# Kernel optimization log

Measured on AMD Instinct MI355X. Metric: run time of the kernel, lower is better.

The kernel has to match this reference:

```python
import jax, jax.numpy as jnp
import numpy as np

B, WIN, DM, DG, K = 32, 128, 1024, 64, 15  # batch, win_size(node feat dim), d_model(#nodes), graph embed, top_k


def setup_inputs() -> dict:
    key = jax.random.key(0)
    ks = jax.random.split(key, 7)
    sc_in = 1.0 / np.sqrt(WIN)
    return {
        "x": jax.random.normal(ks[0], (B, WIN, DM), jnp.float32),
        "Wq": jax.random.normal(ks[1], (DG, WIN), jnp.float32) * sc_in,
        "bq": jax.random.normal(ks[2], (DG,), jnp.float32) * 0.02,
        "Wk": jax.random.normal(ks[3], (DG, WIN), jnp.float32) * sc_in,
        "bk": jax.random.normal(ks[4], (DG,), jnp.float32) * 0.02,
        "Wg": jax.random.normal(ks[5], (WIN, WIN), jnp.float32) * sc_in,  # GCNConv lin weight [out,in]
        "bg": jax.random.normal(ks[6], (WIN,), jnp.float32) * 0.02,
    }


def _gcn_one(nf, Wq, bq, Wk, bk, Wg, bg):
    # nf: [N, F] node features (N = d_model, F = win_size)
    N = nf.shape[0]
    q = nf @ Wq.T + bq                      # [N, DG]
    k = nf @ Wk.T + bk                      # [N, DG]
    scores = (q @ k.T) * (1.0 / np.sqrt(DG))  # [N, N]
    scores = jnp.where(jnp.eye(N, dtype=bool), -jnp.inf, scores)
    _, tgt = jax.lax.top_k(scores, K)       # [N, K] top-k neighbors per source node
    src = jnp.repeat(jnp.arange(N), K)      # [N*K]
    tgt = tgt.reshape(-1)                   # [N*K]
    loops = jnp.arange(N)
    # manual self loops (module) + self loops added internally by GCNConv (default add_self_loops=True)
    src_all = jnp.concatenate([src, loops, loops])
    tgt_all = jnp.concatenate([tgt, loops, loops])
    # gcn_norm: degree over target (col) with unit edge weights
    deg = jax.ops.segment_sum(jnp.ones_like(tgt_all, jnp.float32), tgt_all, num_segments=N)
    dinv = jnp.where(deg > 0, jax.lax.rsqrt(deg), 0.0)
    norm = dinv[src_all] * dinv[tgt_all]    # [E]
    h = nf @ Wg.T                           # [N, F] linear transform (no bias inside lin)
    msg = h[src_all] * norm[:, None]        # gather + scale
    out = jax.ops.segment_sum(msg, tgt_all, num_segments=N) + bg  # scatter-add + bias
    return out                              # [N, F]


def reference(x, Wq, bq, Wk, bk, Wg, bg):
    # x: [B, win_size, d_model] -> nodes: [B, d_model, win_size]
    nodes = x.transpose(0, 2, 1)
    h = jax.vmap(lambda nf: _gcn_one(nf, Wq, bq, Wk, bk, Wg, bg))(nodes)  # [B, N, F]
    # n_layers == 1: no ReLU/dropout applied after last layer
    return h.transpose(0, 2, 1)  # [B, win_size, d_model]
```

## Files before the change

kernel.cpp:

```cpp
#include <hip/hip_runtime.h>

#define NBATCH 32
#define NN     1024
#define NF     128
#define NDG    64
#define TOPK   15

#define OFF_QH    ((size_t)0)
#define OFF_QL    ((size_t)4194304)
#define OFF_KH    ((size_t)8388608)
#define OFF_KL    ((size_t)12582912)
#define OFF_H     ((size_t)16777216)
#define OFF_DEG   ((size_t)33554432)
#define OFF_BMP   ((size_t)33685504)
#define OFF_WL    ((size_t)37879808)
#define OFF_TOPK  ((size_t)38010880)
#define OFF_W64   ((size_t)40108032)
#define OFF_QT64  ((size_t)40239104)
#define OFF_KT64  ((size_t)57016320)
#define OFF_TMP   ((size_t)0)

typedef short s8v  __attribute__((ext_vector_type(8)));
typedef float f4v  __attribute__((ext_vector_type(4)));
typedef unsigned short us8v __attribute__((ext_vector_type(8)));

__device__ inline unsigned short bf16_rne(float f) {
    unsigned u = __float_as_uint(f);
    return (unsigned short)((u + 0x7FFFu + ((u >> 16) & 1u)) >> 16);
}
__device__ inline float bf16_tof(unsigned short h) { return __uint_as_float(((unsigned)h) << 16); }

__device__ inline unsigned pack22(float s) {
    unsigned u   = __float_as_uint(s);
    int      mag = (int)(u & 0x7FFFFFFFu);
    int      t   = mag - 0x38800000;
    t = t < 0 ? 0 : (t > 0x07FFFFFF ? 0x07FFFFFF : t);
    unsigned ts = (unsigned)t >> 6;
    return ((int)u < 0) ? (0x1FFFFFu - ts) : (0x200000u | ts);
}
__device__ inline float dec22(unsigned val22) {
    bool pos = (val22 & 0x200000u) != 0;
    unsigned ts = pos ? (val22 & 0x1FFFFFu) : (0x1FFFFFu - (val22 & 0x1FFFFFu));
    float f = __uint_as_float((ts << 6) + 0x38800000u);
    return pos ? f : -f;
}

__global__ __launch_bounds__(256) void k_upcast(const float* __restrict__ Wq,
                                                const float* __restrict__ Wk,
                                                double* __restrict__ Wq64,
                                                double* __restrict__ Wk64) {
    int i = blockIdx.x * 256 + threadIdx.x;
    Wq64[i] = (double)Wq[i];
    Wk64[i] = (double)Wk[i];
}

__global__ __launch_bounds__(256) void k_prep(
    const float* __restrict__ x, const float* __restrict__ bq, const float* __restrict__ bk,
    const double* __restrict__ Wq64, const double* __restrict__ Wk64,
    const float* __restrict__ Wg,
    unsigned short* __restrict__ qh, unsigned short* __restrict__ ql,
    unsigned short* __restrict__ kh, unsigned short* __restrict__ kl,
    double* __restrict__ qT64, double* __restrict__ kT64,
    float* __restrict__ h,
    uint4* __restrict__ zbase, int zn)
{
    __shared__ float xs[64 * 129];
    const int t = threadIdx.x;
    const int l = t & 63;
    const int w = t >> 6;
    const int uw = __builtin_amdgcn_readfirstlane(w);
    const int n0 = blockIdx.x * 64;
    const int half = blockIdx.y;
    const int b  = blockIdx.z;

    {
        int lid = ((b * 2 + half) * 16 + blockIdx.x) * 256 + t;
        for (int i = lid; i < zn; i += 262144)
            zbase[i] = make_uint4(0u, 0u, 0u, 0u);
    }

    {
        const int j = t & 63, fg = t >> 6;
        for (int ff = 0; ff < 32; ++ff) {
            int f = fg + ff * 4;
            xs[j * 129 + f] = x[((size_t)b * NF + f) * NN + n0 + j];
        }
    }
    __syncthreads();

    {
        const int d0 = half * 32 + uw * 8;
        double accq[8], acck[8];
        #pragma unroll
        for (int dd = 0; dd < 8; ++dd) {
            accq[dd] = (double)bq[d0 + dd];
            acck[dd] = (double)bk[d0 + dd];
        }
        for (int fc = 0; fc < 32; ++fc) {
            double dx0 = (double)xs[l * 129 + fc * 4 + 0];
            double dx1 = (double)xs[l * 129 + fc * 4 + 1];
            double dx2 = (double)xs[l * 129 + fc * 4 + 2];
            double dx3 = (double)xs[l * 129 + fc * 4 + 3];
            #pragma unroll
            for (int dd = 0; dd < 8; ++dd) {
                int d = d0 + dd;
                const double* wq = &Wq64[d * NF + fc * 4];
                const double* wk = &Wk64[d * NF + fc * 4];
                accq[dd] += dx0 * wq[0] + dx1 * wq[1] + dx2 * wq[2] + dx3 * wq[3];
                acck[dd] += dx0 * wk[0] + dx1 * wk[1] + dx2 * wk[2] + dx3 * wk[3];
            }
        }
        #pragma unroll
        for (int dd = 0; dd < 8; ++dd) {
            size_t idx = ((size_t)b * NDG + d0 + dd) * NN + n0 + l;
            qT64[idx] = accq[dd];
            kT64[idx] = acck[dd];
        }
        us8v qh0, ql0, kh0, kl0;
        #pragma unroll
        for (int dd = 0; dd < 8; ++dd) {
            float fq = (float)accq[dd];
            unsigned short h1 = bf16_rne(fq);
            unsigned short l1 = bf16_rne(fq - bf16_tof(h1));
            float fk = (float)acck[dd];
            unsigned short h2 = bf16_rne(fk);
            unsigned short l2 = bf16_rne(fk - bf16_tof(h2));
            qh0[dd] = h1; ql0[dd] = l1; kh0[dd] = h2; kl0[dd] = l2;
        }
        size_t nb = ((size_t)b * NN + n0 + l) * NDG + d0;
        *(us8v*)&qh[nb] = qh0;
        *(us8v*)&ql[nb] = ql0;
        *(us8v*)&kh[nb] = kh0;
        *(us8v*)&kl[nb] = kl0;
    }

    {
        const int fp0 = half * 64 + uw * 16;
        float acc[16];
        #pragma unroll
        for (int i = 0; i < 16; ++i) acc[i] = 0.f;
        for (int fc = 0; fc < 32; ++fc) {
            float x0 = xs[l * 129 + fc * 4 + 0];
            float x1 = xs[l * 129 + fc * 4 + 1];
            float x2 = xs[l * 129 + fc * 4 + 2];
            float x3 = xs[l * 129 + fc * 4 + 3];
            #pragma unroll
            for (int ff = 0; ff < 16; ++ff) {
                const float* wg = &Wg[(fp0 + ff) * NF + fc * 4];
                acc[ff] += x0 * wg[0] + x1 * wg[1] + x2 * wg[2] + x3 * wg[3];
            }
        }
        __syncthreads();
        #pragma unroll
        for (int ff = 0; ff < 16; ++ff) xs[l * 129 + fp0 + ff] = acc[ff];
        __syncthreads();
        for (int r = 0; r < 16; ++r) {
            int idx = t + 256 * r;
            int n = idx >> 6, f = idx & 63;
            h[((size_t)b * NN + n0 + n) * NF + half * 64 + f] = xs[n * 129 + half * 64 + f];
        }
    }
}

__device__ inline unsigned bsort64(unsigned v, int l) {
    #pragma unroll
    for (int k = 2; k <= 64; k <<= 1) {
        #pragma unroll
        for (int j = k >> 1; j >= 1; j >>= 1) {
            unsigned pv = (unsigned)__shfl_xor((int)v, j, 64);
            bool tm = ((l & k) == 0) == ((l & j) == 0);
            unsigned hi = v > pv ? v : pv;
            unsigned lo = v > pv ? pv : v;
            v = tm ? hi : lo;
        }
    }
    return v;
}

__device__ inline void bsort64_2(unsigned& va, unsigned& vb, int l) {
    #pragma unroll
    for (int k = 2; k <= 64; k <<= 1) {
        #pragma unroll
        for (int j = k >> 1; j >= 1; j >>= 1) {
            unsigned pa = (unsigned)__shfl_xor((int)va, j, 64);
            unsigned pb = (unsigned)__shfl_xor((int)vb, j, 64);
            bool tm = ((l & k) == 0) == ((l & j) == 0);
            unsigned ha = va > pa ? va : pa, la = va > pa ? pa : va;
            unsigned hb = vb > pb ? vb : pb, lb = vb > pb ? pb : vb;
            va = tm ? ha : la;
            vb = tm ? hb : lb;
        }
    }
}

__global__ __launch_bounds__(512, 6) void k_score(
    const unsigned short* __restrict__ qh, const unsigned short* __restrict__ ql,
    const unsigned short* __restrict__ kh, const unsigned short* __restrict__ kl,
    const float* __restrict__ bk,
    int* __restrict__ deg, unsigned int* __restrict__ bmp,
    int* __restrict__ topk, int* __restrict__ wl_cnt, int* __restrict__ wl)
{
    __shared__ __align__(16) unsigned slots[16 * 256];
    __shared__ unsigned rowflag[16];
    const int t = threadIdx.x, l = t & 63, w = t >> 6;
    const int b = blockIdx.y, row0 = blockIdx.x * 16;
    const int m = l & 15, q4 = l >> 4;

    {
        uint4* z = (uint4*)slots;
        z[t]       = make_uint4(0u, 0u, 0u, 0u);
        z[t + 512] = make_uint4(0u, 0u, 0u, 0u);
        if (t < 16) rowflag[t] = 0u;
    }

    size_t abase = ((size_t)b * NN + row0 + m) * NDG + q4 * 8;
    s8v ah0 = *(const s8v*)&qh[abase];
    s8v ah1 = *(const s8v*)&qh[abase + 32];
    s8v al0 = *(const s8v*)&ql[abase];
    s8v al1 = *(const s8v*)&ql[abase + 32];

    unsigned Trow[4];
    {
        float ssq = 0.f, smn = 0.f;
        #pragma unroll
        for (int j = 0; j < 8; ++j) {
            float q0 = bf16_tof(((us8v)ah0)[j]) + bf16_tof(((us8v)al0)[j]);
            float q1 = bf16_tof(((us8v)ah1)[j]) + bf16_tof(((us8v)al1)[j]);
            float b0 = bk[q4 * 8 + j];
            float b1 = bk[q4 * 8 + 32 + j];
            ssq += q0 * q0 + q1 * q1;
            smn += q0 * b0 + q1 * b1;
        }
        ssq += __shfl_xor(ssq, 16, 64); ssq += __shfl_xor(ssq, 32, 64);
        smn += __shfl_xor(smn, 16, 64); smn += __shfl_xor(smn, 32, 64);
        float t_m = 0.125f * smn + 0.2125f * __builtin_sqrtf(ssq);
        unsigned Tm = pack22(t_m) << 10;
        #pragma unroll
        for (int r = 0; r < 4; ++r)
            Trow[r] = (unsigned)__shfl((int)Tm, 4 * q4 + r, 64);
    }
    __syncthreads();

    const int colbase = w * 128;
    unsigned basec[4] = {0u, 0u, 0u, 0u};
    #pragma unroll
    for (int tt = 0; tt < 8; ++tt) {
        int col = colbase + tt * 16 + m;
        size_t bbase = ((size_t)b * NN + col) * NDG + q4 * 8;
        s8v bh0 = *(const s8v*)&kh[bbase];
        s8v bh1 = *(const s8v*)&kh[bbase + 32];
        s8v bl0 = *(const s8v*)&kl[bbase];
        s8v bl1 = *(const s8v*)&kl[bbase + 32];
        f4v acc = {0.f, 0.f, 0.f, 0.f};
        acc = __builtin_amdgcn_mfma_f32_16x16x32_bf16(al0, bl0, acc, 0, 0, 0);
        acc = __builtin_amdgcn_mfma_f32_16x16x32_bf16(al1, bl1, acc, 0, 0, 0);
        acc = __builtin_amdgcn_mfma_f32_16x16x32_bf16(ah0, bl0, acc, 0, 0, 0);
        acc = __builtin_amdgcn_mfma_f32_16x16x32_bf16(ah1, bl1, acc, 0, 0, 0);
        acc = __builtin_amdgcn_mfma_f32_16x16x32_bf16(al0, bh0, acc, 0, 0, 0);
        acc = __builtin_amdgcn_mfma_f32_16x16x32_bf16(al1, bh1, acc, 0, 0, 0);
        acc = __builtin_amdgcn_mfma_f32_16x16x32_bf16(ah0, bh0, acc, 0, 0, 0);
        acc = __builtin_amdgcn_mfma_f32_16x16x32_bf16(ah1, bh1, acc, 0, 0, 0);
        #pragma unroll
        for (int r = 0; r < 4; ++r) {
            int row  = q4 * 4 + r;
            int grow = row0 + row;
            float s = acc[r] * 0.125f;
            unsigned c22 = (col == grow) ? 0u : pack22(s);
            unsigned v = (c22 << 10) | (unsigned)(1023 - col);
            bool p = v >= Trow[r];
            unsigned long long mk = __ballot(p);
            unsigned w16 = (unsigned)(mk >> (q4 * 16)) & 0xFFFFu;
            unsigned idx = basec[r] + (unsigned)__popc(w16 & ((1u << m) - 1u));
            if (p && idx < 32u) slots[row * 256 + w * 32 + (int)idx] = v;
            basec[r] += (unsigned)__popc(w16);
        }
    }
    #pragma unroll
    for (int r = 0; r < 4; ++r)
        if (m == 0 && basec[r] > 32u) rowflag[q4 * 4 + r] = 1u;
    __syncthreads();

    const int rA = 2 * w, rB = 2 * w + 1;
    uint4 ca = *(const uint4*)&slots[rA * 256 + l * 4];
    uint4 cb = *(const uint4*)&slots[rB * 256 + l * 4];

    unsigned mxa = ca.x > ca.y ? ca.x : ca.y;  mxa = mxa > ca.z ? mxa : ca.z;  mxa = mxa > ca.w ? mxa : ca.w;
    unsigned mxb = cb.x > cb.y ? cb.x : cb.y;  mxb = mxb > cb.z ? mxb : cb.z;  mxb = mxb > cb.w ? mxb : cb.w;
    bsort64_2(mxa, mxb, l);
    unsigned Ta = (unsigned)__shfl((int)mxa, 15, 64);
    unsigned Tb = (unsigned)__shfl((int)mxb, 15, 64);

    int ka0 = (ca.x >= Ta && ca.x) ? 1 : 0, ka1 = (ca.y >= Ta && ca.y) ? 1 : 0;
    int ka2 = (ca.z >= Ta && ca.z) ? 1 : 0, ka3 = (ca.w >= Ta && ca.w) ? 1 : 0;
    int kb0 = (cb.x >= Tb && cb.x) ? 1 : 0, kb1 = (cb.y >= Tb && cb.y) ? 1 : 0;
    int kb2 = (cb.z >= Tb && cb.z) ? 1 : 0, kb3 = (cb.w >= Tb && cb.w) ? 1 : 0;
    int cntA = ka0 + ka1 + ka2 + ka3;
    int cntB = kb0 + kb1 + kb2 + kb3;
    int preA = cntA, preB = cntB;
    #pragma unroll
    for (int d = 1; d < 64; d <<= 1) {
        int oA = __shfl_up(preA, d, 64);
        int oB = __shfl_up(preB, d, 64);
        if (l >= d) { preA += oA; preB += oB; }
    }
    const int CA = __shfl(preA, 63, 64);
    const int CB = __shfl(preB, 63, 64);

    {
        unsigned* scr = &slots[rA * 256];
        int off = preA - cntA;
        if (ka0) scr[off++] = ca.x;
        if (ka1) scr[off++] = ca.y;
        if (ka2) scr[off++] = ca.z;
        if (ka3) scr[off++] = ca.w;
    }
    {
        unsigned* scr = &slots[rB * 256];
        int off = preB - cntB;
        if (kb0) scr[off++] = cb.x;
        if (kb1) scr[off++] = cb.y;
        if (kb2) scr[off++] = cb.z;
        if (kb3) scr[off++] = cb.w;
    }
    unsigned cva = (l < CA && l < 64) ? slots[rA * 256 + l] : 0u;
    unsigned cvb = (l < CB && l < 64) ? slots[rB * 256 + l] : 0u;
    bsort64_2(cva, cvb, l);

    #pragma unroll
    for (int rr = 0; rr < 2; ++rr) {
        const int row  = rr == 0 ? rA : rB;
        const int grow = row0 + row;
        unsigned res   = rr == 0 ? cva : cvb;
        const int C2   = rr == 0 ? CA : CB;

        unsigned r14 = (unsigned)__shfl((int)res, 14, 64);
        unsigned r15 = (unsigned)__shfl((int)res, 15, 64);
        bool fb = (rowflag[row] != 0u) || (C2 > 64) || (r15 == 0u);

        bool flagged;
        if (fb) {
            flagged = true;
        } else {
            float s15 = dec22(r14 >> 10), s16 = dec22(r15 >> 10);
            unsigned e15 = (__float_as_uint(fabsf(s15)) >> 23) & 255u;
            unsigned e16 = (__float_as_uint(fabsf(s16)) >> 23) & 255u;
            unsigned e = e15 > e16 ? e15 : e16;
            float qq = __uint_as_float((e - 17) << 23);
            flagged = (s15 - s16) < (4.f * qq + 1e-4f);
        }
        if (l < 15) {
            int col = fb ? ((grow + 1 + l) & 1023)
                         : (1023 - (int)(res & 1023u));
            atomicAdd(&deg[b * NN + col], 1);
            atomicOr(&bmp[((size_t)b * NN + col) * 32 + (grow >> 5)], 1u << (grow & 31));
            if (flagged) topk[(b * NN + grow) * 16 + l] = col;
        }
        if (l == 0 && flagged) {
            int idx = atomicAdd(wl_cnt, 1);
            if (idx < 32767) wl[idx] = b * NN + grow;
        }
    }
}

__global__ __launch_bounds__(64) void k_repair(
    const double* __restrict__ qT64, const double* __restrict__ kT64,
    const int* __restrict__ topk, const int* __restrict__ wl_cnt, const int* __restrict__ wl,
    int* __restrict__ deg, unsigned int* __restrict__ bmp)
{
    const int l = threadIdx.x;
    __shared__ double qld[64];
    __shared__ int oldset[15], newset[15];
    const double NEGINF = -__builtin_inf();
    int n = wl_cnt[0]; if (n > 32767) n = 32767;

    for (int i = blockIdx.x; i < n; i += 1024) {
        int rg = wl[i];
        int b = rg >> 10, row = rg & 1023;

        __syncthreads();
        qld[l] = qT64[((size_t)b * NDG + l) * NN + row];
        if (l < 15) oldset[l] = topk[(b * NN + row) * 16 + l];
        __syncthreads();

        double sc[16];
        #pragma unroll
        for (int tt = 0; tt < 16; ++tt) sc[tt] = 0.0;
        const double* kb = &kT64[(size_t)b * NDG * NN];
        double buf[16];
        #pragma unroll
        for (int tt = 0; tt < 16; ++tt) buf[tt] = kb[l + 64 * tt];
        for (int d = 0; d < 64; ++d) {
            double nb[16];
            if (d < 63) {
                const double* kr = kb + (size_t)(d + 1) * NN;
                #pragma unroll
                for (int tt = 0; tt < 16; ++tt) nb[tt] = kr[l + 64 * tt];
            }
            double qd = qld[d];
            #pragma unroll
            for (int tt = 0; tt < 16; ++tt) sc[tt] += qd * buf[tt];
            if (d < 63) {
                #pragma unroll
                for (int tt = 0; tt < 16; ++tt) buf[tt] = nb[tt];
            }
        }
        #pragma unroll
        for (int tt = 0; tt < 16; ++tt) if (l + 64 * tt == row) sc[tt] = NEGINF;

        for (int it = 0; it < 15; ++it) {
            double lv = NEGINF; int lc = 0x7fffffff;
            #pragma unroll
            for (int tt = 0; tt < 16; ++tt)
                if (sc[tt] > lv) { lv = sc[tt]; lc = l + 64 * tt; }
            #pragma unroll
            for (int off = 1; off < 64; off <<= 1) {
                double ov = __shfl_xor(lv, off, 64);
                int    oc = __shfl_xor(lc, off, 64);
                if (ov > lv || (ov == lv && oc < lc)) { lv = ov; lc = oc; }
            }
            #pragma unroll
            for (int tt = 0; tt < 16; ++tt) if (l + 64 * tt == lc) sc[tt] = NEGINF;
            if (l == 0) newset[it] = lc;
        }
        __syncthreads();
        if (l < 15) {
            int cn = newset[l];
            bool found = false;
            #pragma unroll
            for (int j = 0; j < 15; ++j) found = found || (oldset[j] == cn);
            if (!found) {
                atomicAdd(&deg[b * NN + cn], 1);
                atomicOr(&bmp[((size_t)b * NN + cn) * 32 + (row >> 5)], 1u << (row & 31));
            }
            int co = oldset[l];
            found = false;
            #pragma unroll
            for (int j = 0; j < 15; ++j) found = found || (newset[j] == co);
            if (!found) {
                atomicSub(&deg[b * NN + co], 1);
                atomicAnd(&bmp[((size_t)b * NN + co) * 32 + (row >> 5)], ~(1u << (row & 31)));
            }
        }
    }
}

__global__ __launch_bounds__(128) void k_gather(
    const float* __restrict__ h, const float* __restrict__ bg,
    const int* __restrict__ deg, const unsigned int* __restrict__ bmp,
    float* __restrict__ tmp)
{
    __shared__ int list[1024];
    __shared__ float nrm[1024];
    __shared__ int scnt;
    const int tgt = blockIdx.x, b = blockIdx.y, t = threadIdx.x;
    if (t < 32) {
        unsigned word = bmp[((size_t)b * NN + tgt) * 32 + t];
        int pc = __popc(word);
        int pre = pc;
        #pragma unroll
        for (int d = 1; d < 32; d <<= 1) {
            int o = __shfl_up(pre, d, 32);
            if (t >= d) pre += o;
        }
        if (t == 31) scnt = pre;
        int idx = pre - pc;
        while (word) {
            int s = __ffs(word) - 1;
            word &= word - 1;
            list[idx++] = t * 32 + s;
        }
    }
    __syncthreads();
    const int cnt = scnt;
    for (int e = t; e < cnt; e += 128)
        nrm[e] = rsqrtf((float)(deg[b * NN + list[e]] + 2));
    __syncthreads();
    const int f = t;
    float dt = rsqrtf((float)(deg[b * NN + tgt] + 2));
    float acc = 2.0f * dt * h[((size_t)b * NN + tgt) * NF + f];
    for (int e = 0; e < cnt; ++e) {
        int src = list[e];
        acc += h[((size_t)b * NN + src) * NF + f] * nrm[e];
    }
    tmp[((size_t)b * NN + tgt) * NF + f] = bg[f] + dt * acc;
}

__global__ __launch_bounds__(256) void k_transpose(const float* __restrict__ tmp,
                                                   float* __restrict__ out)
{
    __shared__ float tile[32][33];
    const int t = threadIdx.x;
    const int n0 = blockIdx.x * 32, f0 = blockIdx.y * 32, b = blockIdx.z;
    const int c = t & 31, rb = t >> 5;
    #pragma unroll
    for (int i = 0; i < 4; ++i) {
        int r = rb + i * 8;
        tile[r][c] = tmp[((size_t)b * NN + n0 + r) * NF + f0 + c];
    }
    __syncthreads();
    #pragma unroll
    for (int i = 0; i < 4; ++i) {
        int r = rb + i * 8;
        out[((size_t)b * NF + f0 + r) * NN + n0 + c] = tile[c][r];
    }
}

extern "C" void kernel_launch(void* const* d_in, const int* in_sizes, int n_in,
                              void* d_out, int out_size, void* d_ws, size_t ws_size,
                              hipStream_t stream)
{
    const float* x  = (const float*)d_in[0];
    const float* Wq = (const float*)d_in[1];
    const float* bq = (const float*)d_in[2];
    const float* Wk = (const float*)d_in[3];
    const float* bk = (const float*)d_in[4];
    const float* Wg = (const float*)d_in[5];
    const float* bg = (const float*)d_in[6];
    float* out = (float*)d_out;
    char* ws = (char*)d_ws;

    unsigned short* qh = (unsigned short*)(ws + OFF_QH);
    unsigned short* ql = (unsigned short*)(ws + OFF_QL);
    unsigned short* kh = (unsigned short*)(ws + OFF_KH);
    unsigned short* kl = (unsigned short*)(ws + OFF_KL);
    float*          h   = (float*)(ws + OFF_H);
    int*            deg = (int*)(ws + OFF_DEG);
    unsigned int*   bmp = (unsigned int*)(ws + OFF_BMP);
    int*            wlc = (int*)(ws + OFF_WL);
    int*            wl  = wlc + 1;
    int*            tpk = (int*)(ws + OFF_TOPK);
    double*         Wq64 = (double*)(ws + OFF_W64);
    double*         Wk64 = Wq64 + 8192;
    double*         qT64 = (double*)(ws + OFF_QT64);
    double*         kT64 = (double*)(ws + OFF_KT64);
    float*          tmp  = (float*)(ws + OFF_TMP);

    k_upcast<<<32, 256, 0, stream>>>(Wq, Wk, Wq64, Wk64);
    k_prep<<<dim3(16, 2, 32), 256, 0, stream>>>(x, bq, bk, Wq64, Wk64, Wg,
                                                qh, ql, kh, kl, qT64, kT64, h,
                                                (uint4*)(ws + OFF_DEG), 270337);
    k_score<<<dim3(64, 32), 512, 0, stream>>>(qh, ql, kh, kl, bk, deg, bmp, tpk, wlc, wl);
    k_repair<<<1024, 64, 0, stream>>>(qT64, kT64, tpk, wlc, wl, deg, bmp);
    k_gather<<<dim3(1024, 32), 128, 0, stream>>>(h, bg, deg, bmp, tmp);
    k_transpose<<<dim3(32, 4, 32), 256, 0, stream>>>(tmp, out);
}
```

Baseline: 311.2 us.

## Retile top-k scoring kernel, derive degrees from bitmap, unroll gather accumulation

The score kernel now handles 32 rows per 256-thread block. Each wave reuses its K fragments across two row groups and double-buffers the K loads. Candidate slots shrink to 24 per wave, and the per-row count matrix replaces the two-stage max-sort compaction. Degree atomics leave both the score and repair kernels, and a new kernel popcounts the adjacency bitmap to compute degrees. The gather loop uses four independent accumulators. The risks are more fallback rows from the smaller slot capacity and one extra kernel launch.

Measured after the change: 379.8 us. +22.0%, slower.

```diff
diff --git a/kernel.cpp b/kernel.cpp
--- a/kernel.cpp
+++ b/kernel.cpp
@@ -193,39 +193,37 @@
     }
 }
 
-__global__ __launch_bounds__(512, 6) void k_score(
+__global__ __launch_bounds__(256, 4) void k_score(
     const unsigned short* __restrict__ qh, const unsigned short* __restrict__ ql,
     const unsigned short* __restrict__ kh, const unsigned short* __restrict__ kl,
     const float* __restrict__ bk,
-    int* __restrict__ deg, unsigned int* __restrict__ bmp,
+    unsigned int* __restrict__ bmp,
     int* __restrict__ topk, int* __restrict__ wl_cnt, int* __restrict__ wl)
 {
-    __shared__ __align__(16) unsigned slots[16 * 256];
-    __shared__ unsigned rowflag[16];
+    __shared__ unsigned slots[32 * 96];
+    __shared__ int      cntw[32 * 4];
     const int t = threadIdx.x, l = t & 63, w = t >> 6;
-    const int b = blockIdx.y, row0 = blockIdx.x * 16;
+    const int b = blockIdx.y, row0 = blockIdx.x * 32;
     const int m = l & 15, q4 = l >> 4;
 
-    {
-        uint4* z = (uint4*)slots;
-        z[t]       = make_uint4(0u, 0u, 0u, 0u);
-        z[t + 512] = make_uint4(0u, 0u, 0u, 0u);
-        if (t < 16) rowflag[t] = 0u;
-    }
-
-    size_t abase = ((size_t)b * NN + row0 + m) * NDG + q4 * 8;
-    s8v ah0 = *(const s8v*)&qh[abase];
-    s8v ah1 = *(const s8v*)&qh[abase + 32];
-    s8v al0 = *(const s8v*)&ql[abase];
-    s8v al1 = *(const s8v*)&ql[abase + 32];
-
-    unsigned Trow[4];
-    {
+    s8v ah0[2], ah1[2], al0[2], al1[2];
+    #pragma unroll
+    for (int g = 0; g < 2; ++g) {
+        size_t abase = ((size_t)b * NN + row0 + g * 16 + m) * NDG + q4 * 8;
+        ah0[g] = *(const s8v*)&qh[abase];
+        ah1[g] = *(const s8v*)&qh[abase + 32];
+        al0[g] = *(const s8v*)&ql[abase];
+        al1[g] = *(const s8v*)&ql[abase + 32];
+    }
+
+    unsigned Trow[2][4];
+    #pragma unroll
+    for (int g = 0; g < 2; ++g) {
         float ssq = 0.f, smn = 0.f;
         #pragma unroll
         for (int j = 0; j < 8; ++j) {
-            float q0 = bf16_tof(((us8v)ah0)[j]) + bf16_tof(((us8v)al0)[j]);
-            float q1 = bf16_tof(((us8v)ah1)[j]) + bf16_tof(((us8v)al1)[j]);
+            float q0 = bf16_tof(((us8v)ah0[g])[j]) + bf16_tof(((us8v)al0[g])[j]);
+            float q1 = bf16_tof(((us8v)ah1[g])[j]) + bf16_tof(((us8v)al1[g])[j]);
             float b0 = bk[q4 * 8 + j];
             float b1 = bk[q4 * 8 + 32 + j];
             ssq += q0 * q0 + q1 * q1;
@@ -237,127 +235,119 @@
         unsigned Tm = pack22(t_m) << 10;
         #pragma unroll
         for (int r = 0; r < 4; ++r)
-            Trow[r] = (unsigned)__shfl((int)Tm, 4 * q4 + r, 64);
+            Trow[g][r] = (unsigned)__shfl((int)Tm, 4 * q4 + r, 64);
+    }
+
+    const int colbase = w * 256;
+    int basec[2][4] = {{0,0,0,0},{0,0,0,0}};
+
+    s8v Bh0[2], Bh1[2], Bl0[2], Bl1[2];
+    {
+        size_t bb = ((size_t)b * NN + colbase + m) * NDG + q4 * 8;
+        Bh0[0] = *(const s8v*)&kh[bb];
+        Bh1[0] = *(const s8v*)&kh[bb + 32];
+        Bl0[0] = *(const s8v*)&kl[bb];
+        Bl1[0] = *(const s8v*)&kl[bb + 32];
+    }
+    #pragma unroll
+    for (int tt = 0; tt < 16; ++tt) {
+        const int cur = tt & 1;
+        if (tt < 15) {
+            size_t bb = ((size_t)b * NN + colbase + (tt + 1) * 16 + m) * NDG + q4 * 8;
+            Bh0[cur ^ 1] = *(const s8v*)&kh[bb];
+            Bh1[cur ^ 1] = *(const s8v*)&kh[bb + 32];
+            Bl0[cur ^ 1] = *(const s8v*)&kl[bb];
+            Bl1[cur ^ 1] = *(const s8v*)&kl[bb + 32];
+        }
+        const int col = colbase + tt * 16 + m;
+        #pragma unroll
+        for (int g = 0; g < 2; ++g) {
+            f4v acc = {0.f, 0.f, 0.f, 0.f};
+            acc = __builtin_amdgcn_mfma_f32_16x16x32_bf16(al0[g], Bl0[cur], acc, 0, 0, 0);
+            acc = __builtin_amdgcn_mfma_f32_16x16x32_bf16(al1[g], Bl1[cur], acc, 0, 0, 0);
+            acc = __builtin_amdgcn_mfma_f32_16x16x32_bf16(ah0[g], Bl0[cur], acc, 0, 0, 0);
+            acc = __builtin_amdgcn_mfma_f32_16x16x32_bf16(ah1[g], Bl1[cur], acc, 0, 0, 0);
+            acc = __builtin_amdgcn_mfma_f32_16x16x32_bf16(al0[g], Bh0[cur], acc, 0, 0, 0);
+            acc = __builtin_amdgcn_mfma_f32_16x16x32_bf16(al1[g], Bh1[cur], acc, 0, 0, 0);
+            acc = __builtin_amdgcn_mfma_f32_16x16x32_bf16(ah0[g], Bh0[cur], acc, 0, 0, 0);
+            acc = __builtin_amdgcn_mfma_f32_16x16x32_bf16(ah1[g], Bh1[cur], acc, 0, 0, 0);
+            #pragma unroll
+            for (int r = 0; r < 4; ++r) {
+                const int rloc = g * 16 + q4 * 4 + r;
+                const int grow = row0 + rloc;
+                float s = acc[r] * 0.125f;
+                unsigned c22 = (col == grow) ? 0u : pack22(s);
+                unsigned v = (c22 << 10) | (unsigned)(1023 - col);
+                bool p = v >= Trow[g][r];
+                unsigned long long mk = __ballot(p);
+                unsigned w16 = (unsigned)(mk >> (q4 * 16)) & 0xFFFFu;
+                int idx = basec[g][r] + __popc(w16 & ((1u << m) - 1u));
+                if (p && idx < 24) slots[rloc * 96 + w * 24 + idx] = v;
+                basec[g][r] += __popc(w16);
+            }
+        }
+    }
+    if (m == 0) {
+        #pragma unroll
+        for (int g = 0; g < 2; ++g)
+            #pragma unroll
+            for (int r = 0; r < 4; ++r)
+                cntw[(g * 16 + q4 * 4 + r) * 4 + w] = basec[g][r];
     }
     __syncthreads();
 
-    const int colbase = w * 128;
-    unsigned basec[4] = {0u, 0u, 0u, 0u};
-    #pragma unroll
-    for (int tt = 0; tt < 8; ++tt) {
-        int col = colbase + tt * 16 + m;
-        size_t bbase = ((size_t)b * NN + col) * NDG + q4 * 8;
-        s8v bh0 = *(const s8v*)&kh[bbase];
-        s8v bh1 = *(const s8v*)&kh[bbase + 32];
-        s8v bl0 = *(const s8v*)&kl[bbase];
-        s8v bl1 = *(const s8v*)&kl[bbase + 32];
-        f4v acc = {0.f, 0.f, 0.f, 0.f};
-        acc = __builtin_amdgcn_mfma_f32_16x16x32_bf16(al0, bl0, acc, 0, 0, 0);
-        acc = __builtin_amdgcn_mfma_f32_16x16x32_bf16(al1, bl1, acc, 0, 0, 0);
-        acc = __builtin_amdgcn_mfma_f32_16x16x32_bf16(ah0, bl0, acc, 0, 0, 0);
-        acc = __builtin_amdgcn_mfma_f32_16x16x32_bf16(ah1, bl1, acc, 0, 0, 0);
-        acc = __builtin_amdgcn_mfma_f32_16x16x32_bf16(al0, bh0, acc, 0, 0, 0);
-        acc = __builtin_amdgcn_mfma_f32_16x16x32_bf16(al1, bh1, acc, 0, 0, 0);
-        acc = __builtin_amdgcn_mfma_f32_16x16x32_bf16(ah0, bh0, acc, 0, 0, 0);
-        acc = __builtin_amdgcn_mfma_f32_16x16x32_bf16(ah1, bh1, acc, 0, 0, 0);
-        #pragma unroll
-        for (int r = 0; r < 4; ++r) {
-            int row  = q4 * 4 + r;
-            int grow = row0 + row;
-            float s = acc[r] * 0.125f;
-            unsigned c22 = (col == grow) ? 0u : pack22(s);
-            unsigned v = (c22 << 10) | (unsigned)(1023 - col);
-            bool p = v >= Trow[r];
-            unsigned long long mk = __ballot(p);
-            unsigned w16 = (unsigned)(mk >> (q4 * 16)) & 0xFFFFu;
-            unsigned idx = basec[r] + (unsigned)__popc(w16 & ((1u << m) - 1u));
-            if (p && idx < 32u) slots[row * 256 + w * 32 + (int)idx] = v;
-            basec[r] += (unsigned)__popc(w16);
-        }
-    }
-    #pragma unroll
-    for (int r = 0; r < 4; ++r)
-        if (m == 0 && basec[r] > 32u) rowflag[q4 * 4 + r] = 1u;
-    __syncthreads();
-
-    const int rA = 2 * w, rB = 2 * w + 1;
-    uint4 ca = *(const uint4*)&slots[rA * 256 + l * 4];
-    uint4 cb = *(const uint4*)&slots[rB * 256 + l * 4];
-
-    unsigned mxa = ca.x > ca.y ? ca.x : ca.y;  mxa = mxa > ca.z ? mxa : ca.z;  mxa = mxa > ca.w ? mxa : ca.w;
-    unsigned mxb = cb.x > cb.y ? cb.x : cb.y;  mxb = mxb > cb.z ? mxb : cb.z;  mxb = mxb > cb.w ? mxb : cb.w;
-    bsort64_2(mxa, mxb, l);
-    unsigned Ta = (unsigned)__shfl((int)mxa, 15, 64);
-    unsigned Tb = (unsigned)__shfl((int)mxb, 15, 64);
-
-    int ka0 = (ca.x >= Ta && ca.x) ? 1 : 0, ka1 = (ca.y >= Ta && ca.y) ? 1 : 0;
-    int ka2 = (ca.z >= Ta && ca.z) ? 1 : 0, ka3 = (ca.w >= Ta && ca.w) ? 1 : 0;
-    int kb0 = (cb.x >= Tb && cb.x) ? 1 : 0, kb1 = (cb.y >= Tb && cb.y) ? 1 : 0;
-    int kb2 = (cb.z >= Tb && cb.z) ? 1 : 0, kb3 = (cb.w >= Tb && cb.w) ? 1 : 0;
-    int cntA = ka0 + ka1 + ka2 + ka3;
-    int cntB = kb0 + kb1 + kb2 + kb3;
-    int preA = cntA, preB = cntB;
-    #pragma unroll
-    for (int d = 1; d < 64; d <<= 1) {
-        int oA = __shfl_up(preA, d, 64);
-        int oB = __shfl_up(preB, d, 64);
-        if (l >= d) { preA += oA; preB += oB; }
-    }
-    const int CA = __shfl(preA, 63, 64);
-    const int CB = __shfl(preB, 63, 64);
-
-    {
-        unsigned* scr = &slots[rA * 256];
-        int off = preA - cntA;
-        if (ka0) scr[off++] = ca.x;
-        if (ka1) scr[off++] = ca.y;
-        if (ka2) scr[off++] = ca.z;
-        if (ka3) scr[off++] = ca.w;
-    }
-    {
-        unsigned* scr = &slots[rB * 256];
-        int off = preB - cntB;
-        if (kb0) scr[off++] = cb.x;
-        if (kb1) scr[off++] = cb.y;
-        if (kb2) scr[off++] = cb.z;
-        if (kb3) scr[off++] = cb.w;
-    }
-    unsigned cva = (l < CA && l < 64) ? slots[rA * 256 + l] : 0u;
-    unsigned cvb = (l < CB && l < 64) ? slots[rB * 256 + l] : 0u;
-    bsort64_2(cva, cvb, l);
-
-    #pragma unroll
-    for (int rr = 0; rr < 2; ++rr) {
-        const int row  = rr == 0 ? rA : rB;
-        const int grow = row0 + row;
-        unsigned res   = rr == 0 ? cva : cvb;
-        const int C2   = rr == 0 ? CA : CB;
-
-        unsigned r14 = (unsigned)__shfl((int)res, 14, 64);
-        unsigned r15 = (unsigned)__shfl((int)res, 15, 64);
-        bool fb = (rowflag[row] != 0u) || (C2 > 64) || (r15 == 0u);
-
-        bool flagged;
-        if (fb) {
-            flagged = true;
-        } else {
-            float s15 = dec22(r14 >> 10), s16 = dec22(r15 >> 10);
-            unsigned e15 = (__float_as_uint(fabsf(s15)) >> 23) & 255u;
-            unsigned e16 = (__float_as_uint(fabsf(s16)) >> 23) & 255u;
-            unsigned e = e15 > e16 ? e15 : e16;
-            float qq = __uint_as_float((e - 17) << 23);
-            flagged = (s15 - s16) < (4.f * qq + 1e-4f);
-        }
-        if (l < 15) {
-            int col = fb ? ((grow + 1 + l) & 1023)
-                         : (1023 - (int)(res & 1023u));
-            atomicAdd(&deg[b * NN + col], 1);
-            atomicOr(&bmp[((size_t)b * NN + col) * 32 + (grow >> 5)], 1u << (grow & 31));
-            if (flagged) topk[(b * NN + grow) * 16 + l] = col;
-        }
-        if (l == 0 && flagged) {
-            int idx = atomicAdd(wl_cnt, 1);
-            if (idx < 32767) wl[idx] = b * NN + grow;
+    #pragma unroll
+    for (int pp = 0; pp < 4; ++pp) {
+        const int rA = w * 8 + 2 * pp, rB = rA + 1;
+        int a0 = cntw[rA * 4 + 0], a1 = cntw[rA * 4 + 1], a2 = cntw[rA * 4 + 2], a3 = cntw[rA * 4 + 3];
+        int b0 = cntw[rB * 4 + 0], b1 = cntw[rB * 4 + 1], b2 = cntw[rB * 4 + 2], b3 = cntw[rB * 4 + 3];
+        bool ovA = (a0 > 24) || (a1 > 24) || (a2 > 24) || (a3 > 24);
+        bool ovB = (b0 > 24) || (b1 > 24) || (b2 > 24) || (b3 > 24);
+        int rawA = a0 + a1 + a2 + a3, rawB = b0 + b1 + b2 + b3;
+        a0 = a0 > 24 ? 24 : a0; a1 = a1 > 24 ? 24 : a1; a2 = a2 > 24 ? 24 : a2; a3 = a3 > 24 ? 24 : a3;
+        b0 = b0 > 24 ? 24 : b0; b1 = b1 > 24 ? 24 : b1; b2 = b2 > 24 ? 24 : b2; b3 = b3 > 24 ? 24 : b3;
+        int PA1 = a0, PA2 = a0 + a1, PA3 = a0 + a1 + a2, CA = PA3 + a3;
+        int PB1 = b0, PB2 = b0 + b1, PB3 = b0 + b1 + b2, CB = PB3 + b3;
+        bool fbA = ovA || rawA < 16 || rawA > 64;
+        bool fbB = ovB || rawB < 16 || rawB > 64;
+
+        int jA = (l >= PA1) + (l >= PA2) + (l >= PA3);
+        int jB = (l >= PB1) + (l >= PB2) + (l >= PB3);
+        int baseA = jA == 0 ? 0 : (jA == 1 ? PA1 : (jA == 2 ? PA2 : PA3));
+        int baseB = jB == 0 ? 0 : (jB == 1 ? PB1 : (jB == 2 ? PB2 : PB3));
+        unsigned cva = (l < CA) ? slots[rA * 96 + jA * 24 + (l - baseA)] : 0u;
+        unsigned cvb = (l < CB) ? slots[rB * 96 + jB * 24 + (l - baseB)] : 0u;
+        bsort64_2(cva, cvb, l);
+
+        #pragma unroll
+        for (int rr = 0; rr < 2; ++rr) {
+            const int grow = row0 + (rr == 0 ? rA : rB);
+            unsigned res   = rr == 0 ? cva : cvb;
+            const bool fb  = rr == 0 ? fbA : fbB;
+
+            unsigned r14 = (unsigned)__shfl((int)res, 14, 64);
+            unsigned r15 = (unsigned)__shfl((int)res, 15, 64);
+            bool flagged;
+            if (fb) {
+                flagged = true;
+            } else {
+                float s15 = dec22(r14 >> 10), s16 = dec22(r15 >> 10);
+                unsigned e15 = (__float_as_uint(fabsf(s15)) >> 23) & 255u;
+                unsigned e16 = (__float_as_uint(fabsf(s16)) >> 23) & 255u;
+                unsigned e = e15 > e16 ? e15 : e16;
+                float qq = __uint_as_float((e - 17) << 23);
+                flagged = (s15 - s16) < (4.f * qq + 1e-4f);
+            }
+            if (l < 15) {
+                int col = fb ? ((grow + 1 + l) & 1023)
+                             : (1023 - (int)(res & 1023u));
+                atomicOr(&bmp[((size_t)b * NN + col) * 32 + (grow >> 5)], 1u << (grow & 31));
+                if (flagged) topk[(b * NN + grow) * 16 + l] = col;
+            }
+            if (l == 0 && flagged) {
+                int idx = atomicAdd(wl_cnt, 1);
+                if (idx < 32767) wl[idx] = b * NN + grow;
+            }
         }
     }
 }
@@ -365,7 +355,7 @@
 __global__ __launch_bounds__(64) void k_repair(
     const double* __restrict__ qT64, const double* __restrict__ kT64,
     const int* __restrict__ topk, const int* __restrict__ wl_cnt, const int* __restrict__ wl,
-    int* __restrict__ deg, unsigned int* __restrict__ bmp)
+    unsigned int* __restrict__ bmp)
 {
     const int l = threadIdx.x;
     __shared__ double qld[64];
@@ -428,20 +418,30 @@
             bool found = false;
             #pragma unroll
             for (int j = 0; j < 15; ++j) found = found || (oldset[j] == cn);
-            if (!found) {
-                atomicAdd(&deg[b * NN + cn], 1);
+            if (!found)
                 atomicOr(&bmp[((size_t)b * NN + cn) * 32 + (row >> 5)], 1u << (row & 31));
-            }
             int co = oldset[l];
             found = false;
             #pragma unroll
             for (int j = 0; j < 15; ++j) found = found || (newset[j] == co);
-            if (!found) {
-                atomicSub(&deg[b * NN + co], 1);
+            if (!found)
                 atomicAnd(&bmp[((size_t)b * NN + co) * 32 + (row >> 5)], ~(1u << (row & 31)));
-            }
-        }
-    }
+        }
+    }
+}
+
+__global__ __launch_bounds__(256) void k_deg(const unsigned int* __restrict__ bmp,
+                                             int* __restrict__ deg)
+{
+    int i = blockIdx.x * 256 + threadIdx.x;
+    const uint4* p = (const uint4*)(bmp + (size_t)i * 32);
+    int s = 0;
+    #pragma unroll
+    for (int j = 0; j < 8; ++j) {
+        uint4 v = p[j];
+        s += __popc(v.x) + __popc(v.y) + __popc(v.z) + __popc(v.w);
+    }
+    deg[i] = s;
 }
 
 __global__ __launch_bounds__(128) void k_gather(
@@ -477,11 +477,17 @@
     __syncthreads();
     const int f = t;
     float dt = rsqrtf((float)(deg[b * NN + tgt] + 2));
-    float acc = 2.0f * dt * h[((size_t)b * NN + tgt) * NF + f];
-    for (int e = 0; e < cnt; ++e) {
-        int src = list[e];
-        acc += h[((size_t)b * NN + src) * NF + f] * nrm[e];
-    }
+    float a0 = 0.f, a1 = 0.f, a2 = 0.f, a3 = 0.f;
+    int e = 0;
+    for (; e + 4 <= cnt; e += 4) {
+        a0 += h[((size_t)b * NN + list[e + 0]) * NF + f] * nrm[e + 0];
+        a1 += h[((size_t)b * NN + list[e + 1]) * NF + f] * nrm[e + 1];
+        a2 += h[((size_t)b * NN + list[e + 2]) * NF + f] * nrm[e + 2];
+        a3 += h[((size_t)b * NN + list[e + 3]) * NF + f] * nrm[e + 3];
+    }
+    for (; e < cnt; ++e)
+        a0 += h[((size_t)b * NN + list[e]) * NF + f] * nrm[e];
+    float acc = 2.0f * dt * h[((size_t)b * NN + tgt) * NF + f] + ((a0 + a1) + (a2 + a3));
     tmp[((size_t)b * NN + tgt) * NF + f] = bg[f] + dt * acc;
 }
 
@@ -539,8 +545,9 @@
     k_prep<<<dim3(16, 2, 32), 256, 0, stream>>>(x, bq, bk, Wq64, Wk64, Wg,
                                                 qh, ql, kh, kl, qT64, kT64, h,
                                                 (uint4*)(ws + OFF_DEG), 270337);
-    k_score<<<dim3(64, 32), 512, 0, stream>>>(qh, ql, kh, kl, bk, deg, bmp, tpk, wlc, wl);
-    k_repair<<<1024, 64, 0, stream>>>(qT64, kT64, tpk, wlc, wl, deg, bmp);
+    k_score<<<dim3(32, 32), 256, 0, stream>>>(qh, ql, kh, kl, bk, bmp, tpk, wlc, wl);
+    k_repair<<<1024, 64, 0, stream>>>(qT64, kT64, tpk, wlc, wl, bmp);
+    k_deg<<<128, 256, 0, stream>>>(bmp, deg);
     k_gather<<<dim3(1024, 32), 128, 0, stream>>>(h, bg, deg, bmp, tmp);
     k_transpose<<<dim3(32, 4, 32), 256, 0, stream>>>(tmp, out);
 }
```
